# Optimization experiments

Hardware: AMD Instinct MI355X
Metric: run time of the kernel (lower is better)

Reference implementation:

```python
import jax, jax.numpy as jnp
import numpy as np

EPS = 1e-5

def _mode_layer(x, t, w5, w3, w1, a3, a5, gw, gb, gamma, beta):
    # x: [N,Ci,H,W], t: [N,T]
    N = x.shape[0]
    Co = w5.shape[0]
    # gate -> softmax over the 5 experts (dim=1)
    g = t @ gw.T + gb                       # [N, 5*Co]
    g = jax.nn.softmax(g.reshape(N, 5, Co), axis=1)  # [N,5,Co]
    # build the 5 expert kernels, all padded to 5x5 (torch F.pad semantics)
    k3 = jnp.pad(w3, ((0, 0), (0, 0), (1, 1), (1, 1)))
    k1 = jnp.pad(w1, ((0, 0), (0, 0), (2, 2), (2, 2)))
    # avg pool kernels: ones(K,K)/K**3 (faithful to original, incl. the /K^3)
    ka3 = jnp.pad(a3 * (jnp.ones((3, 3), x.dtype) / 27.0), ((0, 0), (0, 0), (1, 1), (1, 1)))
    ka5 = a5 * (jnp.ones((5, 5), x.dtype) / 125.0)
    experts = jnp.stack([w5, k3, k1, ka3, ka5])       # [5,Co,Ci,5,5]
    # per-sample kernels: sum_e g[n,e,o] * experts[e,o,i,h,w]
    w = jnp.einsum('eoihw,neo->noihw', experts, g)    # [N,Co,Ci,5,5]
    # per-sample conv (training-mode path), padding='same', stride=1
    def conv1(xn, wn):
        return jax.lax.conv_general_dilated(xn[None], wn, (1, 1), 'SAME')[0]
    y = jax.vmap(conv1)(x, w)                         # [N,Co,H,W]
    # BatchNorm2d (training mode: biased batch stats) + ReLU
    mean = y.mean(axis=(0, 2, 3))
    var = y.var(axis=(0, 2, 3))
    y = (y - mean[None, :, None, None]) * jax.lax.rsqrt(var + EPS)[None, :, None, None]
    y = y * gamma[None, :, None, None] + beta[None, :, None, None]
    return jax.nn.relu(y)


def setup_inputs() -> dict:
    key = jax.random.key(0)
    ks = jax.random.split(key, 20)
    N, Ci, Co, T, H, W = 8, 32, 64, 8, 256, 256
    f = jnp.float32
    inp = {
        'x': jax.random.normal(ks[0], (N, Ci, H, W), f),
        't': jax.random.normal(ks[1], (N, T), f),
        'w5_1': jax.random.normal(ks[2], (Co, Ci, 5, 5), f) * 0.05,
        'w3_1': jax.random.normal(ks[3], (Co, Ci, 3, 3), f) * 0.05,
        'w1_1': jax.random.normal(ks[4], (Co, Ci, 1, 1), f) * 0.05,
        'a3_1': jax.random.normal(ks[5], (Co, Ci, 1, 1), f) * 0.05,
        'a5_1': jax.random.normal(ks[6], (Co, Ci, 1, 1), f) * 0.05,
        'gw_1': jax.random.normal(ks[7], (5 * Co, T), f) * 0.1,
        'gb_1': jax.random.normal(ks[8], (5 * Co,), f) * 0.1,
        'gamma_1': jnp.ones((Co,), f),
        'beta_1': jnp.zeros((Co,), f),
        'w5_2': jax.random.normal(ks[9], (Co, Co, 5, 5), f) * 0.05,
        'w3_2': jax.random.normal(ks[10], (Co, Co, 3, 3), f) * 0.05,
        'w1_2': jax.random.normal(ks[11], (Co, Co, 1, 1), f) * 0.05,
        'a3_2': jax.random.normal(ks[12], (Co, Co, 1, 1), f) * 0.05,
        'a5_2': jax.random.normal(ks[13], (Co, Co, 1, 1), f) * 0.05,
        'gw_2': jax.random.normal(ks[14], (5 * Co, T), f) * 0.1,
        'gb_2': jax.random.normal(ks[15], (5 * Co,), f) * 0.1,
        'gamma_2': jnp.ones((Co,), f),
        'beta_2': jnp.zeros((Co,), f),
    }
    return inp


def reference(x, t,
              w5_1, w3_1, w1_1, a3_1, a5_1, gw_1, gb_1, gamma_1, beta_1,
              w5_2, w3_2, w1_2, a3_2, a5_2, gw_2, gb_2, gamma_2, beta_2):
    h = _mode_layer(x, t, w5_1, w3_1, w1_1, a3_1, a5_1, gw_1, gb_1, gamma_1, beta_1)
    y = _mode_layer(h, t, w5_2, w3_2, w1_2, a3_2, a5_2, gw_2, gb_2, gamma_2, beta_2)
    return y
```

## Files before the change

kernel.cpp:

```cpp
#include <hip/hip_runtime.h>
#include <hip/hip_bf16.h>

#define MK_N 8
#define MK_T 8
#define MK_H 256
#define MK_W 256
#define MK_CO 64
#define MK_EPS 1e-5f

typedef __attribute__((ext_vector_type(8))) short short8;
typedef __attribute__((ext_vector_type(4))) short short4v;
typedef __attribute__((ext_vector_type(4))) float f32x4;

__device__ __forceinline__ float rdv(const void* p, long idx, int isf32) {
  return isf32 ? ((const float*)p)[idx]
               : __bfloat162float(((const __hip_bfloat16*)p)[idx]);
}

__device__ __forceinline__ short f2bf_s(float f) {
  __hip_bfloat16 b = __float2bfloat16(f);
  union { __hip_bfloat16 b; short s; } u; u.b = b; return u.s;
}
__device__ __forceinline__ float bfu2f(unsigned short s) {
  return __uint_as_float((unsigned)s << 16);
}

__device__ __forceinline__ int block_detect_isf(const void* xprobe, int* sflag) {
  if (threadIdx.x < 64) {
    const unsigned short* u16 = (const unsigned short*)xprobe;
    int insane = 0;
#pragma unroll
    for (int j = 0; j < 4; ++j) {
      unsigned short u = u16[threadIdx.x * 4 + j];
      int e = (u >> 7) & 0xFF;
      bool zero = (u & 0x7FFF) == 0;
      if (!(zero || (e >= 0x60 && e <= 0x85))) insane++;
    }
#pragma unroll
    for (int off = 32; off > 0; off >>= 1) insane += __shfl_down(insane, off);
    if (threadIdx.x == 0) *sflag = (insane > 32) ? 1 : 0;
  }
  __syncthreads();
  return *sflag;
}

__global__ __launch_bounds__(256) void x_to_nhwc(const void* __restrict__ x,
                                                 short* __restrict__ xo,
                                                 const void* __restrict__ xprobe) {
  __shared__ float xl[32 * 65];
  __shared__ int sflag;
  int isf = block_detect_isf(xprobe, &sflag);
  int n = blockIdx.z, y = blockIdx.y, x0 = blockIdx.x * 64;
  int tid = threadIdx.x;
  {
    int c = tid >> 3, ch = tid & 7;
    long base = ((long)(n * 32 + c) * 256 + y) * 256 + x0 + ch * 8;
#pragma unroll
    for (int j = 0; j < 8; ++j) xl[c * 65 + ch * 8 + j] = rdv(x, base + j, isf);
  }
  __syncthreads();
  {
    int xi = tid >> 2, cc = tid & 3;
    short8 v;
#pragma unroll
    for (int j = 0; j < 8; ++j) v[j] = f2bf_s(xl[(cc * 8 + j) * 65 + xi]);
    *(short8*)&xo[(((long)(n * 256 + y) * 256) + x0 + xi) * 32 + cc * 8] = v;
  }
}

__global__ __launch_bounds__(256) void make_panels_dual(
    const void* __restrict__ t,
    const void* __restrict__ gw1, const void* __restrict__ gb1,
    const void* __restrict__ w51, const void* __restrict__ w31,
    const void* __restrict__ w11, const void* __restrict__ a31,
    const void* __restrict__ a51, short* __restrict__ p1,
    const void* __restrict__ gw2, const void* __restrict__ gb2,
    const void* __restrict__ w52, const void* __restrict__ w32,
    const void* __restrict__ w12, const void* __restrict__ a32,
    const void* __restrict__ a52, short* __restrict__ p2,
    const void* __restrict__ xprobe) {
  __shared__ float slog[320], sgate[320];
  __shared__ int sflag;
  const int s = blockIdx.x, n = blockIdx.y, lay = blockIdx.z;
  const int tid = threadIdx.x;
  const int isf = block_detect_isf(xprobe, &sflag);

  const void* gw = lay ? gw2 : gw1;
  const void* gb = lay ? gb2 : gb1;
  const void* w5 = lay ? w52 : w51;
  const void* w3 = lay ? w32 : w31;
  const void* w1 = lay ? w12 : w11;
  const void* a3 = lay ? a32 : a31;
  const void* a5 = lay ? a52 : a51;
  short* pan = lay ? p2 : p1;
  const int CI = lay ? 64 : 32;
  const int HC = CI / 32;

  for (int eo = tid; eo < 320; eo += 256) {
    int e = eo >> 6, o = eo & 63;
    long row = e * 64 + o;
    float sacc = rdv(gb, row, isf);
#pragma unroll
    for (int k = 0; k < MK_T; ++k)
      sacc += rdv(t, n * MK_T + k, isf) * rdv(gw, row * MK_T + k, isf);
    slog[e * 64 + o] = sacc;
  }
  __syncthreads();
  if (tid < 64) {
    float m = slog[tid];
#pragma unroll
    for (int e = 1; e < 5; ++e) m = fmaxf(m, slog[e * 64 + tid]);
    float tmp[5], sum = 0.f;
#pragma unroll
    for (int e = 0; e < 5; ++e) { tmp[e] = expf(slog[e * 64 + tid] - m); sum += tmp[e]; }
    float inv = 1.f / sum;
#pragma unroll
    for (int e = 0; e < 5; ++e) sgate[tid * 5 + e] = tmp[e] * inv;
  }
  __syncthreads();

  const int mo = tid >> 2, gq = tid & 3;
  float ge[5];
#pragma unroll
  for (int e = 0; e < 5; ++e) ge[e] = sgate[mo * 5 + e];

  const int ky = s / 5, kx = s - ky * 5;
  const bool in3 = (ky >= 1 && ky <= 3 && kx >= 1 && kx <= 3);
  for (int hc = 0; hc < HC; ++hc) {
    short8 pk;
#pragma unroll
    for (int j = 0; j < 8; ++j) {
      long oc = (long)mo * CI + hc * 32 + gq * 8 + j;
      float pa3 = rdv(a3, oc, isf) * (1.f / 27.f);
      float pa5 = rdv(a5, oc, isf) * (1.f / 125.f);
      float v = ge[0] * rdv(w5, oc * 25 + s, isf);
      if (in3) {
        v += ge[1] * rdv(w3, oc * 9 + (ky - 1) * 3 + (kx - 1), isf);
        v += ge[3] * pa3;
      }
      if (s == 12) v += ge[2] * rdv(w1, oc, isf);
      v += ge[4] * pa5;
      pk[j] = f2bf_s(v);
    }
    *(short8*)&pan[((((long)n * HC + hc) * 25 + s) * 64 + mo) * 32 + gq * 8] = pk;
  }
}

__global__ __launch_bounds__(256) void copy16(const short8* __restrict__ src,
                                              short8* __restrict__ dst, int n16) {
  int i = blockIdx.x * 256 + threadIdx.x;
  if (i < n16) dst[i] = src[i];
}

__global__ __launch_bounds__(256) void reduce_finalize(
    const float* __restrict__ part, int nb,
    const float* __restrict__ stin, float* __restrict__ stout,
    float* __restrict__ params,
    const void* __restrict__ gamma, const void* __restrict__ beta,
    const void* __restrict__ xprobe) {
  __shared__ float rs[256], rq[256];
  __shared__ int sflag;
  const int isf = block_detect_isf(xprobe, &sflag);
  const int o = blockIdx.x;
  const int tid = threadIdx.x;
  float s = 0.f, q = 0.f;
  for (int k = tid; k < nb; k += 256) {
    s += part[(long)o * nb + k];
    q += part[(long)(64 + o) * nb + k];
  }
  rs[tid] = s; rq[tid] = q;
  __syncthreads();
  if (tid < 64) {
    s = rs[tid] + rs[tid + 64] + rs[tid + 128] + rs[tid + 192];
    q = rq[tid] + rq[tid + 64] + rq[tid + 128] + rq[tid + 192];
#pragma unroll
    for (int off = 32; off > 0; off >>= 1) {
      s += __shfl_down(s, off);
      q += __shfl_down(q, off);
    }
    if (tid == 0) {
      if (stin) { s += stin[o]; q += stin[64 + o]; }
      if (stout) { stout[o] = s; stout[64 + o] = q; }
      if (params) {
        const float M = (float)(MK_N * MK_H * MK_W);
        float mean = s / M;
        float var = q / M - mean * mean;
        float inv = rsqrtf(var + MK_EPS);
        float sc = rdv(gamma, o, isf) * inv;
        params[o] = sc;
        params[MK_CO + o] = rdv(beta, o, isf) - mean * sc;
      }
    }
  }
}

template <int CI, bool FINAL, bool BNIN>
__global__ __launch_bounds__(256, 2) void conv_mfma(
    const short* __restrict__ xsrc,
    const short* __restrict__ pan,
    void* __restrict__ outp,
    int nbase,
    const float* __restrict__ pr,
    float* __restrict__ partials,
    int NB)
{
  constexpr int XT_SH = FINAL ? 29376 : 37888;
  __shared__ short xt[XT_SH];
  __shared__ float spr[128];

  const int tid = threadIdx.x;
  const int x0 = blockIdx.x * 64;
  const int r0 = blockIdx.y * 8;
  const int n = blockIdx.z + nbase;
  const int bid = (blockIdx.z * gridDim.y + blockIdx.y) * gridDim.x + blockIdx.x;

  if (BNIN) {
    if (tid < 128) spr[tid] = pr[tid];
  }

  const int lane = tid & 63, w = tid >> 6;
  const int quad = lane >> 4, l15 = lane & 15;

  int baseB[2][4];
#pragma unroll
  for (int rr = 0; rr < 2; ++rr)
#pragma unroll
    for (int p = 0; p < 4; ++p)
      baseB[rr][p] = ((w + rr * 4) * 68 + p * 16 + l15) * 36 + quad * 8;
  int aoff[4];
#pragma unroll
  for (int ot = 0; ot < 4; ++ot)
    aoff[ot] = (ot * 16 + l15) * 32 + quad * 8;

  f32x4 acc[2][4][4];
#pragma unroll
  for (int rr = 0; rr < 2; ++rr)
#pragma unroll
    for (int ot = 0; ot < 4; ++ot)
#pragma unroll
      for (int p = 0; p < 4; ++p) acc[rr][ot][p] = f32x4{0.f, 0.f, 0.f, 0.f};

  const int HC = CI / 32;
#pragma unroll 1
  for (int hc = 0; hc < HC; ++hc) {
    const int cbase = hc * 32;
    __syncthreads();

    for (int idx = tid; idx < 12 * 68 * 4; idx += 256) {
      int r = idx / (68 * 4);
      int rem = idx - r * (68 * 4);
      int col = rem >> 2, ch = rem & 3;
      int gy = r0 - 2 + r, gx = x0 - 2 + col;
      short8 v = short8{0, 0, 0, 0, 0, 0, 0, 0};
      if ((unsigned)gy < 256u && (unsigned)gx < 256u) {
        v = *(const short8*)&xsrc[(((long)(n * 256 + gy) * 256) + gx) * CI + cbase + ch * 8];
        if (BNIN) {
#pragma unroll
          for (int j = 0; j < 8; ++j) {
            int c = cbase + ch * 8 + j;
            float f = bfu2f((unsigned short)v[j]);
            v[j] = f2bf_s(fmaxf(fmaf(f, spr[c], spr[64 + c]), 0.f));
          }
        }
      }
      short4v lo, hi;
#pragma unroll
      for (int j = 0; j < 4; ++j) { lo[j] = v[j]; hi[j] = v[4 + j]; }
      int sb = (r * 68 + col) * 36 + ch * 8;
      *(short4v*)&xt[sb] = lo;
      *(short4v*)&xt[sb + 4] = hi;
    }
    __syncthreads();

    const short* ps = pan + (((long)n * HC + hc) * 25) * 2048;

    short8 afc[4], afn[4];
#pragma unroll
    for (int ot = 0; ot < 4; ++ot) {
      afc[ot] = *(const short8*)&ps[aoff[ot]];
      afn[ot] = *(const short8*)&ps[2048 + aoff[ot]];
    }

#pragma unroll
    for (int s = 0; s < 25; ++s) {
      const int ky = s / 5, kx = s - ky * 5;
      const int koff = (ky * 68 + kx) * 36;
      short8 af2[4];
      if (s < 23) {
#pragma unroll
        for (int ot = 0; ot < 4; ++ot)
          af2[ot] = *(const short8*)&ps[(s + 2) * 2048 + aoff[ot]];
      }
      short8 bf[2][4];
#pragma unroll
      for (int rr = 0; rr < 2; ++rr)
#pragma unroll
        for (int p = 0; p < 4; ++p) {
          short4v lo = *(const short4v*)&xt[baseB[rr][p] + koff];
          short4v hi = *(const short4v*)&xt[baseB[rr][p] + koff + 4];
          short8 b;
#pragma unroll
          for (int j = 0; j < 4; ++j) { b[j] = lo[j]; b[4 + j] = hi[j]; }
          bf[rr][p] = b;
        }
      __builtin_amdgcn_s_setprio(1);
#pragma unroll
      for (int ot = 0; ot < 4; ++ot)
#pragma unroll
        for (int rr = 0; rr < 2; ++rr)
#pragma unroll
          for (int p = 0; p < 4; ++p)
            acc[rr][ot][p] = __builtin_amdgcn_mfma_f32_16x16x32_bf16(
                afc[ot], bf[rr][p], acc[rr][ot][p], 0, 0, 0);
      __builtin_amdgcn_s_setprio(0);
      if (s < 24) {
#pragma unroll
        for (int ot = 0; ot < 4; ++ot) {
          afc[ot] = afn[ot];
          if (s < 23) afn[ot] = af2[ot];
        }
      }
    }
  }

  float* slds = FINAL ? (float*)xt : (float*)&xt[36864];

  if (FINAL) {
    float* out = (float*)outp;
#pragma unroll
    for (int rr = 0; rr < 2; ++rr)
#pragma unroll
      for (int ot = 0; ot < 4; ++ot)
#pragma unroll
        for (int p = 0; p < 4; ++p)
#pragma unroll
          for (int r = 0; r < 4; ++r) {
            int oo = ot * 16 + quad * 4 + r;
            long off = ((long)(n * 64 + oo) << 16) + (r0 + w + rr * 4) * 256 + x0 + p * 16 + l15;
            out[off] = acc[rr][ot][p][r];
          }
    __syncthreads();
#pragma unroll
    for (int ot = 0; ot < 4; ++ot)
#pragma unroll
      for (int r = 0; r < 4; ++r) {
        float s = 0.f, q = 0.f;
#pragma unroll
        for (int rr = 0; rr < 2; ++rr)
#pragma unroll
          for (int p = 0; p < 4; ++p) {
            float v = acc[rr][ot][p][r];
            s += v; q += v * v;
          }
#pragma unroll
        for (int m = 1; m < 16; m <<= 1) {
          s += __shfl_xor(s, m);
          q += __shfl_xor(q, m);
        }
        if (l15 == 0) {
          int ch = ot * 16 + quad * 4 + r;
          slds[w * 128 + ch] = s;
          slds[w * 128 + 64 + ch] = q;
        }
      }
    __syncthreads();
    if (tid < 128) {
      float v = slds[tid] + slds[128 + tid] + slds[256 + tid] + slds[384 + tid];
      partials[(long)tid * NB + bid] = v;
    }
  } else {
    __syncthreads();
    short* cbuf = xt;
#pragma unroll
    for (int rr = 0; rr < 2; ++rr)
#pragma unroll
      for (int ot = 0; ot < 4; ++ot)
#pragma unroll
        for (int p = 0; p < 4; ++p) {
          short4v pk;
#pragma unroll
          for (int r = 0; r < 4; ++r) pk[r] = f2bf_s(acc[rr][ot][p][r]);
          *(short4v*)&cbuf[((w + rr * 4) * 64 + p * 16 + l15) * 72 + ot * 16 + quad * 4] = pk;
        }
#pragma unroll
    for (int ot = 0; ot < 4; ++ot)
#pragma unroll
      for (int r = 0; r < 4; ++r) {
        float s = 0.f, q = 0.f;
#pragma unroll
        for (int rr = 0; rr < 2; ++rr)
#pragma unroll
          for (int p = 0; p < 4; ++p) {
            float v = acc[rr][ot][p][r];
            s += v; q += v * v;
          }
#pragma unroll
        for (int m = 1; m < 16; m <<= 1) {
          s += __shfl_xor(s, m);
          q += __shfl_xor(q, m);
        }
        if (l15 == 0) {
          int ch = ot * 16 + quad * 4 + r;
          slds[w * 128 + ch] = s;
          slds[w * 128 + 64 + ch] = q;
        }
      }
    __syncthreads();
    short* hout = (short*)outp;
    for (int idx = tid; idx < 4096; idx += 256) {
      int w2 = idx >> 9, rem = idx & 511;
      int px = rem >> 3, ch = rem & 7;
      short8 v = *(const short8*)&cbuf[(w2 * 64 + px) * 72 + ch * 8];
      *(short8*)&hout[(((long)(n * 256 + r0 + w2) * 256) + x0 + px) * 64 + ch * 8] = v;
    }
    if (tid < 128) {
      float v = slds[tid] + slds[128 + tid] + slds[256 + tid] + slds[384 + tid];
      partials[(long)tid * NB + bid] = v;
    }
  }
}

__global__ __launch_bounds__(256) void bn_relu_f32v(float4* __restrict__ y,
                                                    const float* __restrict__ params) {
  const long total = (long)MK_N * MK_CO * MK_H * MK_W / 4;
  for (long i = (long)blockIdx.x * 256 + threadIdx.x; i < total;
       i += (long)gridDim.x * 256) {
    int ch = (int)((i >> 14) & (MK_CO - 1));
    float sc = params[ch], sh = params[MK_CO + ch];
    float4 v = y[i];
    v.x = fmaxf(fmaf(v.x, sc, sh), 0.f);
    v.y = fmaxf(fmaf(v.y, sc, sh), 0.f);
    v.z = fmaxf(fmaf(v.z, sc, sh), 0.f);
    v.w = fmaxf(fmaf(v.w, sc, sh), 0.f);
    y[i] = v;
  }
}

extern "C" void kernel_launch(void* const* d_in, const int* in_sizes, int n_in,
                              void* d_out, int out_size, void* d_ws, size_t ws_size,
                              hipStream_t stream) {
  const void* x     = d_in[0];
  const void* t     = d_in[1];
  const void* w5_1  = d_in[2];
  const void* w3_1  = d_in[3];
  const void* w1_1  = d_in[4];
  const void* a3_1  = d_in[5];
  const void* a5_1  = d_in[6];
  const void* gw_1  = d_in[7];
  const void* gb_1  = d_in[8];
  const void* gamma_1 = d_in[9];
  const void* beta_1  = d_in[10];
  const void* w5_2  = d_in[11];
  const void* w3_2  = d_in[12];
  const void* w1_2  = d_in[13];
  const void* a3_2  = d_in[14];
  const void* a5_2  = d_in[15];
  const void* gw_2  = d_in[16];
  const void* gb_2  = d_in[17];
  const void* gamma_2 = d_in[18];
  const void* beta_2  = d_in[19];

  char* dob = (char*)d_out;
  short* x_nhwc = (short*)d_out;
  float* part1 = (float*)(dob + 33554432 + 4096);
  short* P1    = (short*)(dob + 35651584);
  short* P2    = (short*)(dob + 104857600);
  float* pr1_hi = (float*)(dob + 104857600 + 1638400);
  float* part2a = (float*)(dob + 132120576);
  float* out = (float*)d_out;

  char* wsb = (char*)d_ws;
  short* h     = (short*)d_ws;
  float* st2   = (float*)d_ws;
  float* pr2   = st2 + 128;
  float* part2b = (float*)(wsb + 4096);
  short* P2c   = (short*)(wsb + 2097152);
  float* pr1c  = (float*)(wsb + 2097152 + 1638400);

  make_panels_dual<<<dim3(25, 8, 2), 256, 0, stream>>>(
      t, gw_1, gb_1, w5_1, w3_1, w1_1, a3_1, a5_1, P1,
      gw_2, gb_2, w5_2, w3_2, w1_2, a3_2, a5_2, P2, x);

  x_to_nhwc<<<dim3(4, 256, 8), 256, 0, stream>>>(x, x_nhwc, x);
  conv_mfma<32, false, false><<<dim3(4, 32, 8), 256, 0, stream>>>(
      x_nhwc, P1, h, 0, nullptr, part1, 1024);
  reduce_finalize<<<64, 256, 0, stream>>>(part1, 1024, nullptr, nullptr,
                                          pr1_hi, gamma_1, beta_1, x);

  conv_mfma<64, true, true><<<dim3(4, 32, 4), 256, 0, stream>>>(
      h, P2, out, 0, pr1_hi, part2a, 512);
  reduce_finalize<<<64, 256, 0, stream>>>(part2a, 512, nullptr, st2,
                                          nullptr, nullptr, nullptr, x);
  copy16<<<401, 256, 0, stream>>>((const short8*)P2, (short8*)P2c, 102432);
  conv_mfma<64, true, true><<<dim3(4, 32, 4), 256, 0, stream>>>(
      h, P2c, out, 4, pr1c, part2b, 512);
  reduce_finalize<<<64, 256, 0, stream>>>(part2b, 512, st2, nullptr,
                                          pr2, gamma_2, beta_2, x);
  bn_relu_f32v<<<2048, 256, 0, stream>>>((float4*)out, pr2);
}
```

Before: 458.4 us.

## Fuse NCHW-to-NHWC conversion into first conv tile load and shorten A-prefetch

Removes the separate x_to_nhwc kernel and has the first conv read NCHW input directly, converting to bf16 and transposing into the shared-memory tile. This drops one full write and read of the converted input. The trade is a scalar-ish LDS store pattern with per-element 2-byte writes, plus a dtype probe inside the conv. The weight-panel prefetch depth is also cut from two steps ahead to one to save registers, and the bn_relu grid size is doubled.

```diff
diff --git a/kernel.cpp b/kernel.cpp
--- a/kernel.cpp
+++ b/kernel.cpp
@@ -42,30 +42,6 @@
   }
   __syncthreads();
   return *sflag;
-}
-
-__global__ __launch_bounds__(256) void x_to_nhwc(const void* __restrict__ x,
-                                                 short* __restrict__ xo,
-                                                 const void* __restrict__ xprobe) {
-  __shared__ float xl[32 * 65];
-  __shared__ int sflag;
-  int isf = block_detect_isf(xprobe, &sflag);
-  int n = blockIdx.z, y = blockIdx.y, x0 = blockIdx.x * 64;
-  int tid = threadIdx.x;
-  {
-    int c = tid >> 3, ch = tid & 7;
-    long base = ((long)(n * 32 + c) * 256 + y) * 256 + x0 + ch * 8;
-#pragma unroll
-    for (int j = 0; j < 8; ++j) xl[c * 65 + ch * 8 + j] = rdv(x, base + j, isf);
-  }
-  __syncthreads();
-  {
-    int xi = tid >> 2, cc = tid & 3;
-    short8 v;
-#pragma unroll
-    for (int j = 0; j < 8; ++j) v[j] = f2bf_s(xl[(cc * 8 + j) * 65 + xi]);
-    *(short8*)&xo[(((long)(n * 256 + y) * 256) + x0 + xi) * 32 + cc * 8] = v;
-  }
 }
 
 __global__ __launch_bounds__(256) void make_panels_dual(
@@ -194,9 +170,10 @@
   }
 }
 
-template <int CI, bool FINAL, bool BNIN>
+template <int CI, bool FINAL, bool BNIN, bool NCHW>
 __global__ __launch_bounds__(256, 2) void conv_mfma(
-    const short* __restrict__ xsrc,
+    const void* __restrict__ xsrc,
+    const void* __restrict__ xprobe,
     const short* __restrict__ pan,
     void* __restrict__ outp,
     int nbase,
@@ -207,6 +184,7 @@
   constexpr int XT_SH = FINAL ? 29376 : 37888;
   __shared__ short xt[XT_SH];
   __shared__ float spr[128];
+  __shared__ int sflag;
 
   const int tid = threadIdx.x;
   const int x0 = blockIdx.x * 64;
@@ -214,6 +192,9 @@
   const int n = blockIdx.z + nbase;
   const int bid = (blockIdx.z * gridDim.y + blockIdx.y) * gridDim.x + blockIdx.x;
 
+  int isf = 0;
+  if (NCHW) isf = block_detect_isf(xprobe, &sflag);
+
   if (BNIN) {
     if (tid < 128) spr[tid] = pr[tid];
   }
@@ -246,50 +227,84 @@
     const int cbase = hc * 32;
     __syncthreads();
 
-    for (int idx = tid; idx < 12 * 68 * 4; idx += 256) {
-      int r = idx / (68 * 4);
-      int rem = idx - r * (68 * 4);
-      int col = rem >> 2, ch = rem & 3;
-      int gy = r0 - 2 + r, gx = x0 - 2 + col;
-      short8 v = short8{0, 0, 0, 0, 0, 0, 0, 0};
-      if ((unsigned)gy < 256u && (unsigned)gx < 256u) {
-        v = *(const short8*)&xsrc[(((long)(n * 256 + gy) * 256) + gx) * CI + cbase + ch * 8];
-        if (BNIN) {
-#pragma unroll
-          for (int j = 0; j < 8; ++j) {
-            int c = cbase + ch * 8 + j;
-            float f = bfu2f((unsigned short)v[j]);
-            v[j] = f2bf_s(fmaxf(fmaf(f, spr[c], spr[64 + c]), 0.f));
+    if (NCHW) {
+      for (int idx = tid; idx < 32 * 12 * 18; idx += 256) {
+        int c = idx / 216;
+        int rem = idx - c * 216;
+        int r = rem / 18, g = rem - r * 18;
+        int gy = r0 - 2 + r;
+        int gx0 = x0 - 4 + g * 4;
+        long base = ((long)(n * 32 + c) * 256 + gy) * 256 + gx0;
+        float f[4];
+        bool rowok = (unsigned)gy < 256u;
+        if (rowok && gx0 >= 0 && gx0 + 3 < 256) {
+          if (isf) {
+            float4 v = *(const float4*)((const float*)xsrc + base);
+            f[0] = v.x; f[1] = v.y; f[2] = v.z; f[3] = v.w;
+          } else {
+            short4v v = *(const short4v*)((const short*)xsrc + base);
+#pragma unroll
+            for (int j = 0; j < 4; ++j) f[j] = bfu2f((unsigned short)v[j]);
           }
-        }
-      }
-      short4v lo, hi;
-#pragma unroll
-      for (int j = 0; j < 4; ++j) { lo[j] = v[j]; hi[j] = v[4 + j]; }
-      int sb = (r * 68 + col) * 36 + ch * 8;
-      *(short4v*)&xt[sb] = lo;
-      *(short4v*)&xt[sb + 4] = hi;
+        } else if (rowok) {
+#pragma unroll
+          for (int j = 0; j < 4; ++j) {
+            int gx = gx0 + j;
+            f[j] = ((unsigned)gx < 256u) ? rdv(xsrc, base + j, isf) : 0.f;
+          }
+        } else {
+          f[0] = f[1] = f[2] = f[3] = 0.f;
+        }
+#pragma unroll
+        for (int j = 0; j < 4; ++j) {
+          int col = g * 4 + j - 2;
+          if ((unsigned)col < 68u) xt[(r * 68 + col) * 36 + c] = f2bf_s(f[j]);
+        }
+      }
+    } else {
+      const short* xs = (const short*)xsrc;
+      for (int idx = tid; idx < 12 * 68 * 4; idx += 256) {
+        int r = idx / (68 * 4);
+        int rem = idx - r * (68 * 4);
+        int col = rem >> 2, ch = rem & 3;
+        int gy = r0 - 2 + r, gx = x0 - 2 + col;
+        short8 v = short8{0, 0, 0, 0, 0, 0, 0, 0};
+        if ((unsigned)gy < 256u && (unsigned)gx < 256u) {
+          v = *(const short8*)&xs[(((long)(n * 256 + gy) * 256) + gx) * CI + cbase + ch * 8];
+          if (BNIN) {
+#pragma unroll
+            for (int j = 0; j < 8; ++j) {
+              int c = cbase + ch * 8 + j;
+              float f = bfu2f((unsigned short)v[j]);
+              v[j] = f2bf_s(fmaxf(fmaf(f, spr[c], spr[64 + c]), 0.f));
+            }
+          }
+        }
+        short4v lo, hi;
+#pragma unroll
+        for (int j = 0; j < 4; ++j) { lo[j] = v[j]; hi[j] = v[4 + j]; }
+        int sb = (r * 68 + col) * 36 + ch * 8;
+        *(short4v*)&xt[sb] = lo;
+        *(short4v*)&xt[sb + 4] = hi;
+      }
     }
     __syncthreads();
 
     const short* ps = pan + (((long)n * HC + hc) * 25) * 2048;
 
-    short8 afc[4], afn[4];
-#pragma unroll
-    for (int ot = 0; ot < 4; ++ot) {
-      afc[ot] = *(const short8*)&ps[aoff[ot]];
-      afn[ot] = *(const short8*)&ps[2048 + aoff[ot]];
-    }
+    short8 afc[4];
+#pragma unroll
+    for (int ot = 0; ot < 4; ++ot) afc[ot] = *(const short8*)&ps[aoff[ot]];
 
 #pragma unroll
     for (int s = 0; s < 25; ++s) {
       const int ky = s / 5, kx = s - ky * 5;
       const int koff = (ky * 68 + kx) * 36;
-      short8 af2[4];
-      if (s < 23) {
+      short8 afn[4];
+      if (s < 24) {
 #pragma unroll
         for (int ot = 0; ot < 4; ++ot)
-          af2[ot] = *(const short8*)&ps[(s + 2) * 2048 + aoff[ot]];
+          afn[ot] = *(const short8*)&ps[(s + 1) * 2048 + aoff[ot]];
       }
       short8 bf[2][4];
 #pragma unroll
@@ -315,10 +330,7 @@
       __builtin_amdgcn_s_setprio(0);
       if (s < 24) {
 #pragma unroll
-        for (int ot = 0; ot < 4; ++ot) {
-          afc[ot] = afn[ot];
-          if (s < 23) afn[ot] = af2[ot];
-        }
+        for (int ot = 0; ot < 4; ++ot) afc[ot] = afn[ot];
       }
     }
   }
@@ -461,7 +473,6 @@
   const void* beta_2  = d_in[19];
 
   char* dob = (char*)d_out;
-  short* x_nhwc = (short*)d_out;
   float* part1 = (float*)(dob + 33554432 + 4096);
   short* P1    = (short*)(dob + 35651584);
   short* P2    = (short*)(dob + 104857600);
@@ -481,20 +492,19 @@
       t, gw_1, gb_1, w5_1, w3_1, w1_1, a3_1, a5_1, P1,
       gw_2, gb_2, w5_2, w3_2, w1_2, a3_2, a5_2, P2, x);
 
-  x_to_nhwc<<<dim3(4, 256, 8), 256, 0, stream>>>(x, x_nhwc, x);
-  conv_mfma<32, false, false><<<dim3(4, 32, 8), 256, 0, stream>>>(
-      x_nhwc, P1, h, 0, nullptr, part1, 1024);
+  conv_mfma<32, false, false, true><<<dim3(4, 32, 8), 256, 0, stream>>>(
+      x, x, P1, h, 0, nullptr, part1, 1024);
   reduce_finalize<<<64, 256, 0, stream>>>(part1, 1024, nullptr, nullptr,
                                           pr1_hi, gamma_1, beta_1, x);
 
-  conv_mfma<64, true, true><<<dim3(4, 32, 4), 256, 0, stream>>>(
-      h, P2, out, 0, pr1_hi, part2a, 512);
+  conv_mfma<64, true, true, false><<<dim3(4, 32, 4), 256, 0, stream>>>(
+      h, x, P2, out, 0, pr1_hi, part2a, 512);
   reduce_finalize<<<64, 256, 0, stream>>>(part2a, 512, nullptr, st2,
                                           nullptr, nullptr, nullptr, x);
   copy16<<<401, 256, 0, stream>>>((const short8*)P2, (short8*)P2c, 102432);
-  conv_mfma<64, true, true><<<dim3(4, 32, 4), 256, 0, stream>>>(
-      h, P2c, out, 4, pr1c, part2b, 512);
+  conv_mfma<64, true, true, false><<<dim3(4, 32, 4), 256, 0, stream>>>(
+      h, x, P2c, out, 4, pr1c, part2b, 512);
   reduce_finalize<<<64, 256, 0, stream>>>(part2b, 512, st2, nullptr,
                                           pr2, gamma_2, beta_2, x);
-  bn_relu_f32v<<<2048, 256, 0, stream>>>((float4*)out, pr2);
-}
+  bn_relu_f32v<<<4096, 256, 0, stream>>>((float4*)out, pr2);
+}
```

Measured after the change: 436.9 us. -4.7%, faster.
